# Kernel tuning notes

Hardware: AMD Instinct MI355X
Metric: run time of the kernel (lower is better)

Reference implementation:

```python
import jax, jax.numpy as jnp
import numpy as np

B, L, D, E, He = 8, 512, 300, 64, 64  # batch, seq_len, hidden_dim, edge_embed_dim, edge_hidden_dim


def setup_inputs() -> dict:
    key = jax.random.key(0)
    ks = jax.random.split(key, 7)
    return {
        "x": jax.random.normal(ks[0], (B, L, D), jnp.float32),
        "adj": jax.random.randint(ks[1], (B, L, L), 0, 2).astype(jnp.int32),
        "edge_embedding": jax.random.normal(ks[2], (B, L, L, E), jnp.float32),
        # learned params (xavier-ish scaling)
        "W_map": jax.random.normal(ks[3], (E, He), jnp.float32) / np.sqrt(E).astype(np.float32),
        "w_ew": jax.random.normal(ks[4], (He, 1), jnp.float32) / np.sqrt(He).astype(np.float32),
        "W_eto": jax.random.normal(ks[5], (D, D), jnp.float32) / np.sqrt(D).astype(np.float32),
        "b_eto": jnp.zeros((D,), jnp.float32),
    }


def reference(x, adj, edge_embedding, W_map, w_ew, W_eto, b_eto):
    # edge_mapping -> relu (dropout is identity in eval mode)
    em = jax.nn.relu(jnp.einsum('bije,eh->bijh', edge_embedding, W_map))  # [B,L,L,He]
    # edge_weight_liner (bias-free) -> [B,L,L]
    ew = jnp.einsum('bijh,ho->bij', em, w_ew)
    # row-wise abs-mean normalization (torch: mean(dim=-1).unsqueeze(-1), + 1e-10)
    row_mean = jnp.abs(jnp.mean(ew, axis=-1, keepdims=True)) + 1e-10
    ew = ew / row_mean
    # adjacency-masked softmax (torch uses -9e15 fill)
    scores = jnp.where(adj != 0, ew, jnp.float32(-9e15))
    att = jax.nn.softmax(scores, axis=-1)  # [B,L,L]
    # dense aggregation: edge_to(input) then attention matmul, relu
    h = x @ W_eto + b_eto  # [B,L,D]
    h_edge = jax.nn.relu(jnp.einsum('bij,bjd->bid', att, h))  # [B,L,D]
    return h_edge, att
```

## Files before the change

### kernel.cpp

```cpp
#include <hip/hip_runtime.h>
#include <hip/hip_bf16.h>

#define LSEQ 512
#define DDIM 300

typedef __attribute__((ext_vector_type(8))) short short8;
typedef __attribute__((ext_vector_type(4))) float f32x4;

__device__ __forceinline__ void split4(f32x4 v, short8& hi, short8& lo, int base) {
  #pragma unroll
  for (int e = 0; e < 4; ++e) {
    const float f = v[e];
    const unsigned b = __float_as_uint(f);
    const float hf = __uint_as_float(b & 0xffff0000u);
    hi[base + e] = (short)(b >> 16);
    lo[base + e] = (short)(__float_as_uint(f - hf) >> 16);
  }
}

__global__ __launch_bounds__(256, 3) void k_ew(
    const float* __restrict__ emb, const float* __restrict__ Wmap,
    const float* __restrict__ wew, float* __restrict__ ew) {
  __shared__ float lds[2][4][1024];
  const int tid = threadIdx.x;
  const int lane = tid & 63, wid = tid >> 6;
  const int c = lane & 15, g = lane >> 4;

  short8 whi[4][2], wlo[4][2];
  #pragma unroll
  for (int nt = 0; nt < 4; ++nt) {
    #pragma unroll
    for (int s = 0; s < 2; ++s) {
      #pragma unroll
      for (int e2 = 0; e2 < 2; ++e2) {
        f32x4 w;
        #pragma unroll
        for (int e = 0; e < 4; ++e)
          w[e] = Wmap[(32 * s + 8 * g + 4 * e2 + e) * 64 + 16 * nt + c];
        split4(w, whi[nt][s], wlo[nt][s], 4 * e2);
      }
    }
  }
  float wv2[4][4];
  #pragma unroll
  for (int nt = 0; nt < 4; ++nt)
    #pragma unroll
    for (int reg = 0; reg < 4; ++reg)
      wv2[nt][reg] = wew[16 * nt + 4 * g + reg];

  const size_t ebase = ((size_t)blockIdx.x * 4 + wid) * 128;
  const float* gbase = emb + (ebase << 6);

  float* const lb0 = &lds[0][wid][0];
  float* const lb1 = &lds[1][wid][0];

  int wwb[4];
  #pragma unroll
  for (int i = 0; i < 4; ++i)
    wwb[i] = ((i * 1024 + lane * 16) ^ ((((i & 1) * 4 + g) & 7) << 4)) >> 2;

  const int rw0 = (c * 256 + (((2 * g + 0) ^ (c & 7)) << 4)) >> 2;
  const int rw1 = (c * 256 + (((2 * g + 1) ^ (c & 7)) << 4)) >> 2;
  const int rw2 = (c * 256 + (((2 * g + 8) ^ (c & 7)) << 4)) >> 2;
  const int rw3 = (c * 256 + (((2 * g + 9) ^ (c & 7)) << 4)) >> 2;

  f32x4 q0 = *(const f32x4*)(gbase + 0 * 256 + lane * 4);
  f32x4 q1 = *(const f32x4*)(gbase + 1 * 256 + lane * 4);
  f32x4 q2 = *(const f32x4*)(gbase + 2 * 256 + lane * 4);
  f32x4 q3 = *(const f32x4*)(gbase + 3 * 256 + lane * 4);
  *(f32x4*)(lb0 + wwb[0]) = q0;
  *(f32x4*)(lb0 + wwb[1]) = q1;
  *(f32x4*)(lb0 + wwb[2]) = q2;
  *(f32x4*)(lb0 + wwb[3]) = q3;

  #pragma unroll 1
  for (int it = 0; it < 8; ++it) {
    if (it < 7) {
      const float* nt_ = gbase + (size_t)(it + 1) * 1024;
      q0 = *(const f32x4*)(nt_ + 0 * 256 + lane * 4);
      q1 = *(const f32x4*)(nt_ + 1 * 256 + lane * 4);
      q2 = *(const f32x4*)(nt_ + 2 * 256 + lane * 4);
      q3 = *(const f32x4*)(nt_ + 3 * 256 + lane * 4);
    }
    float* const rb = (it & 1) ? lb1 : lb0;
    const f32x4 a0 = *(const f32x4*)(rb + rw0);
    const f32x4 a1 = *(const f32x4*)(rb + rw1);
    const f32x4 a2 = *(const f32x4*)(rb + rw2);
    const f32x4 a3 = *(const f32x4*)(rb + rw3);

    short8 ehi[2], elo[2];
    split4(a0, ehi[0], elo[0], 0);
    split4(a1, ehi[0], elo[0], 4);
    split4(a2, ehi[1], elo[1], 0);
    split4(a3, ehi[1], elo[1], 4);

    f32x4 acc[4];
    #pragma unroll
    for (int nt = 0; nt < 4; ++nt) acc[nt] = (f32x4){0.f, 0.f, 0.f, 0.f};
    #pragma unroll
    for (int s = 0; s < 2; ++s) {
      #pragma unroll
      for (int nt = 0; nt < 4; ++nt) {
        acc[nt] = __builtin_amdgcn_mfma_f32_16x16x32_bf16(whi[nt][s], ehi[s], acc[nt], 0, 0, 0);
        acc[nt] = __builtin_amdgcn_mfma_f32_16x16x32_bf16(whi[nt][s], elo[s], acc[nt], 0, 0, 0);
        acc[nt] = __builtin_amdgcn_mfma_f32_16x16x32_bf16(wlo[nt][s], ehi[s], acc[nt], 0, 0, 0);
      }
    }
    float p = 0.f;
    #pragma unroll
    for (int nt = 0; nt < 4; ++nt)
      #pragma unroll
      for (int reg = 0; reg < 4; ++reg)
        p = fmaf(fmaxf(acc[nt][reg], 0.f), wv2[nt][reg], p);
    p += __shfl_xor(p, 16, 64);
    p += __shfl_xor(p, 32, 64);
    if (lane < 16) ew[ebase + it * 16 + c] = p;

    if (it < 7) {
      float* const wb = (it & 1) ? lb0 : lb1;
      *(f32x4*)(wb + wwb[0]) = q0;
      *(f32x4*)(wb + wwb[1]) = q1;
      *(f32x4*)(wb + wwb[2]) = q2;
      *(f32x4*)(wb + wwb[3]) = q3;
    }
  }
}

__global__ __launch_bounds__(256) void k_sm(
    const float* __restrict__ ew, const int* __restrict__ adj,
    float* __restrict__ att) {
  __shared__ float redA[4], redB[4], redC[4];
  const int tid = threadIdx.x;
  const int lane = tid & 63, wid = tid >> 6;
  const size_t rowbase = (size_t)blockIdx.x * LSEQ;

  const float ew0 = ew[rowbase + tid];
  const float ew1 = ew[rowbase + tid + 256];

  float ls = ew0 + ew1;
  #pragma unroll
  for (int m = 32; m >= 1; m >>= 1) ls += __shfl_xor(ls, m, 64);
  if (lane == 0) redA[wid] = ls;
  __syncthreads();
  const float rmean =
      fabsf((redA[0] + redA[1] + redA[2] + redA[3]) * (1.0f / 512.0f)) + 1e-10f;

  const int a0i = adj[rowbase + tid];
  const int a1i = adj[rowbase + tid + 256];
  const float sc0 = a0i ? (ew0 / rmean) : -9e15f;
  const float sc1 = a1i ? (ew1 / rmean) : -9e15f;

  float lm = fmaxf(sc0, sc1);
  #pragma unroll
  for (int m = 32; m >= 1; m >>= 1) lm = fmaxf(lm, __shfl_xor(lm, m, 64));
  if (lane == 0) redB[wid] = lm;
  __syncthreads();
  const float mx = fmaxf(fmaxf(redB[0], redB[1]), fmaxf(redB[2], redB[3]));

  const float e0 = expf(sc0 - mx);
  const float e1 = expf(sc1 - mx);
  float es = e0 + e1;
  #pragma unroll
  for (int m = 32; m >= 1; m >>= 1) es += __shfl_xor(es, m, 64);
  if (lane == 0) redC[wid] = es;
  __syncthreads();
  const float denom = redC[0] + redC[1] + redC[2] + redC[3];

  att[rowbase + tid] = e0 / denom;
  att[rowbase + tid + 256] = e1 / denom;
}

__global__ __launch_bounds__(256) void k_h(
    const float* __restrict__ x, const float* __restrict__ W,
    const float* __restrict__ bias, float* __restrict__ h) {
  const int tid = threadIdx.x;
  const int lane = tid & 63, wid = tid >> 6;
  const int c = lane & 15, g = lane >> 4;
  const int gt = blockIdx.x * 4 + wid;
  const int rt = gt / 19, dt = gt % 19;
  const int r0 = rt * 16, d0 = dt * 16;
  const int dc = min(d0 + c, DDIM - 1);
  const float* xr = x + (size_t)(r0 + c) * DDIM;

  f32x4 acc = {0.f, 0.f, 0.f, 0.f};
  #pragma unroll 3
  for (int ks = 0; ks < 9; ++ks) {
    const int k0 = ks * 32 + 8 * g;
    const f32x4 a0 = *(const f32x4*)(xr + k0);
    const f32x4 a1 = *(const f32x4*)(xr + k0 + 4);
    short8 ahi, alo;
    split4(a0, ahi, alo, 0);
    split4(a1, ahi, alo, 4);
    const float* wp = W + (size_t)k0 * DDIM + dc;
    const f32x4 b0 = {wp[0], wp[DDIM], wp[2 * DDIM], wp[3 * DDIM]};
    const f32x4 b1 = {wp[4 * DDIM], wp[5 * DDIM], wp[6 * DDIM], wp[7 * DDIM]};
    short8 bhi, blo;
    split4(b0, bhi, blo, 0);
    split4(b1, bhi, blo, 4);
    acc = __builtin_amdgcn_mfma_f32_16x16x32_bf16(ahi, bhi, acc, 0, 0, 0);
    acc = __builtin_amdgcn_mfma_f32_16x16x32_bf16(ahi, blo, acc, 0, 0, 0);
    acc = __builtin_amdgcn_mfma_f32_16x16x32_bf16(alo, bhi, acc, 0, 0, 0);
  }
  {
    float av[8], bv[8];
    #pragma unroll
    for (int e = 0; e < 8; ++e) {
      const int kk = 288 + 8 * g + e;
      const bool ok = kk < DDIM;
      av[e] = ok ? xr[kk] : 0.f;
      bv[e] = ok ? W[(size_t)kk * DDIM + dc] : 0.f;
    }
    const f32x4 a0 = {av[0], av[1], av[2], av[3]};
    const f32x4 a1 = {av[4], av[5], av[6], av[7]};
    const f32x4 b0 = {bv[0], bv[1], bv[2], bv[3]};
    const f32x4 b1 = {bv[4], bv[5], bv[6], bv[7]};
    short8 ahi, alo, bhi, blo;
    split4(a0, ahi, alo, 0);
    split4(a1, ahi, alo, 4);
    split4(b0, bhi, blo, 0);
    split4(b1, bhi, blo, 4);
    acc = __builtin_amdgcn_mfma_f32_16x16x32_bf16(ahi, bhi, acc, 0, 0, 0);
    acc = __builtin_amdgcn_mfma_f32_16x16x32_bf16(ahi, blo, acc, 0, 0, 0);
    acc = __builtin_amdgcn_mfma_f32_16x16x32_bf16(alo, bhi, acc, 0, 0, 0);
  }
  if (d0 + c < DDIM) {
    const float bb = bias[d0 + c];
    #pragma unroll
    for (int reg = 0; reg < 4; ++reg)
      h[(size_t)(r0 + 4 * g + reg) * DDIM + d0 + c] = acc[reg] + bb;
  }
}

__global__ __launch_bounds__(256) void k_out(
    const float* __restrict__ att, const float* __restrict__ h,
    float* __restrict__ out) {
  const int tid = threadIdx.x;
  const int lane = tid & 63, wid = tid >> 6;
  const int c = lane & 15, g = lane >> 4;
  const int gt = blockIdx.x * 4 + wid;
  const int b = gt / 608, rem = gt % 608;
  const int it = rem / 19, dt = rem % 19;
  const int i0 = it * 16, d0 = dt * 16;
  const int dc = min(d0 + c, DDIM - 1);
  const float* attR = att + ((size_t)b * LSEQ + i0 + c) * LSEQ + 8 * g;
  const float* hB = h + (size_t)b * LSEQ * DDIM;

  f32x4 acc = {0.f, 0.f, 0.f, 0.f};
  #pragma unroll 2
  for (int ks = 0; ks < 16; ++ks) {
    const int k0 = ks * 32;
    const f32x4 a0 = *(const f32x4*)(attR + k0);
    const f32x4 a1 = *(const f32x4*)(attR + k0 + 4);
    short8 ahi, alo;
    split4(a0, ahi, alo, 0);
    split4(a1, ahi, alo, 4);
    const float* hp = hB + (size_t)(k0 + 8 * g) * DDIM + dc;
    const f32x4 b0 = {hp[0], hp[DDIM], hp[2 * DDIM], hp[3 * DDIM]};
    const f32x4 b1 = {hp[4 * DDIM], hp[5 * DDIM], hp[6 * DDIM], hp[7 * DDIM]};
    short8 bhi, blo;
    split4(b0, bhi, blo, 0);
    split4(b1, bhi, blo, 4);
    acc = __builtin_amdgcn_mfma_f32_16x16x32_bf16(ahi, bhi, acc, 0, 0, 0);
    acc = __builtin_amdgcn_mfma_f32_16x16x32_bf16(ahi, blo, acc, 0, 0, 0);
    acc = __builtin_amdgcn_mfma_f32_16x16x32_bf16(alo, bhi, acc, 0, 0, 0);
  }
  if (d0 + c < DDIM) {
    #pragma unroll
    for (int reg = 0; reg < 4; ++reg)
      out[((size_t)b * LSEQ + i0 + 4 * g + reg) * DDIM + d0 + c] =
          fmaxf(acc[reg], 0.f);
  }
}

extern "C" void kernel_launch(void* const* d_in, const int* in_sizes, int n_in,
                              void* d_out, int out_size, void* d_ws, size_t ws_size,
                              hipStream_t stream) {
  const float* x    = (const float*)d_in[0];
  const int*   adj  = (const int*)d_in[1];
  const float* emb  = (const float*)d_in[2];
  const float* Wmap = (const float*)d_in[3];
  const float* wew  = (const float*)d_in[4];
  const float* Weto = (const float*)d_in[5];
  const float* beto = (const float*)d_in[6];

  float* out    = (float*)d_out;
  float* h_edge = out;
  float* att    = out + (size_t)8 * LSEQ * DDIM;
  float* ew     = (float*)d_ws;
  float* h      = ew + (size_t)8 * LSEQ * LSEQ;

  k_ew<<<dim3(4096), 256, 0, stream>>>(emb, Wmap, wew, ew);
  k_sm<<<dim3(4096), 256, 0, stream>>>(ew, adj, att);
  k_h<<<dim3(1216), 256, 0, stream>>>(x, Weto, beto, h);
  k_out<<<dim3(1216), 256, 0, stream>>>(att, h, h_edge);
}
```

Measured before the change: 160.8 us.

## Fuse edge-weight, softmax and h projection into one kernel; widen k_out tile

```diff
diff --git a/kernel.cpp b/kernel.cpp
--- a/kernel.cpp
+++ b/kernel.cpp
@@ -18,13 +18,75 @@
   }
 }
 
-__global__ __launch_bounds__(256, 3) void k_ew(
-    const float* __restrict__ emb, const float* __restrict__ Wmap,
-    const float* __restrict__ wew, float* __restrict__ ew) {
-  __shared__ float lds[2][4][1024];
+__global__ __launch_bounds__(256, 3) void k_fused1(
+    const float* __restrict__ emb, const int* __restrict__ adj,
+    const float* __restrict__ Wmap, const float* __restrict__ wew,
+    const float* __restrict__ x, const float* __restrict__ Weto,
+    const float* __restrict__ beto,
+    float* __restrict__ att, float* __restrict__ h) {
+  __shared__ float stg[2][4][1024];
+  __shared__ float ew_lds[LSEQ];
+  __shared__ float redA[4], redB[4], redC[4];
   const int tid = threadIdx.x;
   const int lane = tid & 63, wid = tid >> 6;
   const int c = lane & 15, g = lane >> 4;
+
+  if (blockIdx.x >= 4096) {
+    const int gt = (blockIdx.x - 4096) * 4 + wid;
+    const int rt = gt / 19, dt = gt % 19;
+    const int r0 = rt * 16, d0 = dt * 16;
+    const int dc = min(d0 + c, DDIM - 1);
+    const float* xr = x + (size_t)(r0 + c) * DDIM;
+
+    f32x4 acc = {0.f, 0.f, 0.f, 0.f};
+    #pragma unroll 3
+    for (int ks = 0; ks < 9; ++ks) {
+      const int k0 = ks * 32 + 8 * g;
+      const f32x4 a0 = *(const f32x4*)(xr + k0);
+      const f32x4 a1 = *(const f32x4*)(xr + k0 + 4);
+      short8 ahi, alo;
+      split4(a0, ahi, alo, 0);
+      split4(a1, ahi, alo, 4);
+      const float* wp = Weto + (size_t)k0 * DDIM + dc;
+      const f32x4 b0 = {wp[0], wp[DDIM], wp[2 * DDIM], wp[3 * DDIM]};
+      const f32x4 b1 = {wp[4 * DDIM], wp[5 * DDIM], wp[6 * DDIM], wp[7 * DDIM]};
+      short8 bhi, blo;
+      split4(b0, bhi, blo, 0);
+      split4(b1, bhi, blo, 4);
+      acc = __builtin_amdgcn_mfma_f32_16x16x32_bf16(ahi, bhi, acc, 0, 0, 0);
+      acc = __builtin_amdgcn_mfma_f32_16x16x32_bf16(ahi, blo, acc, 0, 0, 0);
+      acc = __builtin_amdgcn_mfma_f32_16x16x32_bf16(alo, bhi, acc, 0, 0, 0);
+    }
+    {
+      float av[8], bv[8];
+      #pragma unroll
+      for (int e = 0; e < 8; ++e) {
+        const int kk = 288 + 8 * g + e;
+        const bool ok = kk < DDIM;
+        av[e] = ok ? xr[kk] : 0.f;
+        bv[e] = ok ? Weto[(size_t)kk * DDIM + dc] : 0.f;
+      }
+      const f32x4 a0 = {av[0], av[1], av[2], av[3]};
+      const f32x4 a1 = {av[4], av[5], av[6], av[7]};
+      const f32x4 b0 = {bv[0], bv[1], bv[2], bv[3]};
+      const f32x4 b1 = {bv[4], bv[5], bv[6], bv[7]};
+      short8 ahi, alo, bhi, blo;
+      split4(a0, ahi, alo, 0);
+      split4(a1, ahi, alo, 4);
+      split4(b0, bhi, blo, 0);
+      split4(b1, bhi, blo, 4);
+      acc = __builtin_amdgcn_mfma_f32_16x16x32_bf16(ahi, bhi, acc, 0, 0, 0);
+      acc = __builtin_amdgcn_mfma_f32_16x16x32_bf16(ahi, blo, acc, 0, 0, 0);
+      acc = __builtin_amdgcn_mfma_f32_16x16x32_bf16(alo, bhi, acc, 0, 0, 0);
+    }
+    if (d0 + c < DDIM) {
+      const float bb = beto[d0 + c];
+      #pragma unroll
+      for (int reg = 0; reg < 4; ++reg)
+        h[(size_t)(r0 + 4 * g + reg) * DDIM + d0 + c] = acc[reg] + bb;
+    }
+    return;
+  }
 
   short8 whi[4][2], wlo[4][2];
   #pragma unroll
@@ -48,11 +110,12 @@
     for (int reg = 0; reg < 4; ++reg)
       wv2[nt][reg] = wew[16 * nt + 4 * g + reg];
 
-  const size_t ebase = ((size_t)blockIdx.x * 4 + wid) * 128;
+  const size_t rowbase = (size_t)blockIdx.x * LSEQ;
+  const size_t ebase = rowbase + (size_t)wid * 128;
   const float* gbase = emb + (ebase << 6);
 
-  float* const lb0 = &lds[0][wid][0];
-  float* const lb1 = &lds[1][wid][0];
+  float* const lb0 = &stg[0][wid][0];
+  float* const lb1 = &stg[1][wid][0];
 
   int wwb[4];
   #pragma unroll
@@ -114,7 +177,7 @@
         p = fmaf(fmaxf(acc[nt][reg], 0.f), wv2[nt][reg], p);
     p += __shfl_xor(p, 16, 64);
     p += __shfl_xor(p, 32, 64);
-    if (lane < 16) ew[ebase + it * 16 + c] = p;
+    if (lane < 16) ew_lds[wid * 128 + it * 16 + c] = p;
 
     if (it < 7) {
       float* const wb = (it & 1) ? lb0 : lb1;
@@ -124,18 +187,10 @@
       *(f32x4*)(wb + wwb[3]) = q3;
     }
   }
-}
-
-__global__ __launch_bounds__(256) void k_sm(
-    const float* __restrict__ ew, const int* __restrict__ adj,
-    float* __restrict__ att) {
-  __shared__ float redA[4], redB[4], redC[4];
-  const int tid = threadIdx.x;
-  const int lane = tid & 63, wid = tid >> 6;
-  const size_t rowbase = (size_t)blockIdx.x * LSEQ;
-
-  const float ew0 = ew[rowbase + tid];
-  const float ew1 = ew[rowbase + tid + 256];
+  __syncthreads();
+
+  const float ew0 = ew_lds[tid];
+  const float ew1 = ew_lds[tid + 256];
 
   float ls = ew0 + ew1;
   #pragma unroll
@@ -168,67 +223,6 @@
 
   att[rowbase + tid] = e0 / denom;
   att[rowbase + tid + 256] = e1 / denom;
-}
-
-__global__ __launch_bounds__(256) void k_h(
-    const float* __restrict__ x, const float* __restrict__ W,
-    const float* __restrict__ bias, float* __restrict__ h) {
-  const int tid = threadIdx.x;
-  const int lane = tid & 63, wid = tid >> 6;
-  const int c = lane & 15, g = lane >> 4;
-  const int gt = blockIdx.x * 4 + wid;
-  const int rt = gt / 19, dt = gt % 19;
-  const int r0 = rt * 16, d0 = dt * 16;
-  const int dc = min(d0 + c, DDIM - 1);
-  const float* xr = x + (size_t)(r0 + c) * DDIM;
-
-  f32x4 acc = {0.f, 0.f, 0.f, 0.f};
-  #pragma unroll 3
-  for (int ks = 0; ks < 9; ++ks) {
-    const int k0 = ks * 32 + 8 * g;
-    const f32x4 a0 = *(const f32x4*)(xr + k0);
-    const f32x4 a1 = *(const f32x4*)(xr + k0 + 4);
-    short8 ahi, alo;
-    split4(a0, ahi, alo, 0);
-    split4(a1, ahi, alo, 4);
-    const float* wp = W + (size_t)k0 * DDIM + dc;
-    const f32x4 b0 = {wp[0], wp[DDIM], wp[2 * DDIM], wp[3 * DDIM]};
-    const f32x4 b1 = {wp[4 * DDIM], wp[5 * DDIM], wp[6 * DDIM], wp[7 * DDIM]};
-    short8 bhi, blo;
-    split4(b0, bhi, blo, 0);
-    split4(b1, bhi, blo, 4);
-    acc = __builtin_amdgcn_mfma_f32_16x16x32_bf16(ahi, bhi, acc, 0, 0, 0);
-    acc = __builtin_amdgcn_mfma_f32_16x16x32_bf16(ahi, blo, acc, 0, 0, 0);
-    acc = __builtin_amdgcn_mfma_f32_16x16x32_bf16(alo, bhi, acc, 0, 0, 0);
-  }
-  {
-    float av[8], bv[8];
-    #pragma unroll
-    for (int e = 0; e < 8; ++e) {
-      const int kk = 288 + 8 * g + e;
-      const bool ok = kk < DDIM;
-      av[e] = ok ? xr[kk] : 0.f;
-      bv[e] = ok ? W[(size_t)kk * DDIM + dc] : 0.f;
-    }
-    const f32x4 a0 = {av[0], av[1], av[2], av[3]};
-    const f32x4 a1 = {av[4], av[5], av[6], av[7]};
-    const f32x4 b0 = {bv[0], bv[1], bv[2], bv[3]};
-    const f32x4 b1 = {bv[4], bv[5], bv[6], bv[7]};
-    short8 ahi, alo, bhi, blo;
-    split4(a0, ahi, alo, 0);
-    split4(a1, ahi, alo, 4);
-    split4(b0, bhi, blo, 0);
-    split4(b1, bhi, blo, 4);
-    acc = __builtin_amdgcn_mfma_f32_16x16x32_bf16(ahi, bhi, acc, 0, 0, 0);
-    acc = __builtin_amdgcn_mfma_f32_16x16x32_bf16(ahi, blo, acc, 0, 0, 0);
-    acc = __builtin_amdgcn_mfma_f32_16x16x32_bf16(alo, bhi, acc, 0, 0, 0);
-  }
-  if (d0 + c < DDIM) {
-    const float bb = bias[d0 + c];
-    #pragma unroll
-    for (int reg = 0; reg < 4; ++reg)
-      h[(size_t)(r0 + 4 * g + reg) * DDIM + d0 + c] = acc[reg] + bb;
-  }
 }
 
 __global__ __launch_bounds__(256) void k_out(
@@ -238,37 +232,49 @@
   const int lane = tid & 63, wid = tid >> 6;
   const int c = lane & 15, g = lane >> 4;
   const int gt = blockIdx.x * 4 + wid;
-  const int b = gt / 608, rem = gt % 608;
-  const int it = rem / 19, dt = rem % 19;
-  const int i0 = it * 16, d0 = dt * 16;
+  const int b = gt / 304, rem = gt % 304;
+  const int i2 = rem / 19, dt = rem % 19;
+  const int i0 = i2 * 32, d0 = dt * 16;
   const int dc = min(d0 + c, DDIM - 1);
-  const float* attR = att + ((size_t)b * LSEQ + i0 + c) * LSEQ + 8 * g;
+  const float* attR0 = att + ((size_t)b * LSEQ + i0 + c) * LSEQ + 8 * g;
+  const float* attR1 = attR0 + (size_t)16 * LSEQ;
   const float* hB = h + (size_t)b * LSEQ * DDIM;
 
-  f32x4 acc = {0.f, 0.f, 0.f, 0.f};
+  f32x4 acc0 = {0.f, 0.f, 0.f, 0.f};
+  f32x4 acc1 = {0.f, 0.f, 0.f, 0.f};
   #pragma unroll 2
   for (int ks = 0; ks < 16; ++ks) {
     const int k0 = ks * 32;
-    const f32x4 a0 = *(const f32x4*)(attR + k0);
-    const f32x4 a1 = *(const f32x4*)(attR + k0 + 4);
-    short8 ahi, alo;
-    split4(a0, ahi, alo, 0);
-    split4(a1, ahi, alo, 4);
+    const f32x4 a0 = *(const f32x4*)(attR0 + k0);
+    const f32x4 a1 = *(const f32x4*)(attR0 + k0 + 4);
+    const f32x4 a2 = *(const f32x4*)(attR1 + k0);
+    const f32x4 a3 = *(const f32x4*)(attR1 + k0 + 4);
+    short8 ahi0, alo0, ahi1, alo1;
+    split4(a0, ahi0, alo0, 0);
+    split4(a1, ahi0, alo0, 4);
+    split4(a2, ahi1, alo1, 0);
+    split4(a3, ahi1, alo1, 4);
     const float* hp = hB + (size_t)(k0 + 8 * g) * DDIM + dc;
     const f32x4 b0 = {hp[0], hp[DDIM], hp[2 * DDIM], hp[3 * DDIM]};
     const f32x4 b1 = {hp[4 * DDIM], hp[5 * DDIM], hp[6 * DDIM], hp[7 * DDIM]};
     short8 bhi, blo;
     split4(b0, bhi, blo, 0);
     split4(b1, bhi, blo, 4);
-    acc = __builtin_amdgcn_mfma_f32_16x16x32_bf16(ahi, bhi, acc, 0, 0, 0);
-    acc = __builtin_amdgcn_mfma_f32_16x16x32_bf16(ahi, blo, acc, 0, 0, 0);
-    acc = __builtin_amdgcn_mfma_f32_16x16x32_bf16(alo, bhi, acc, 0, 0, 0);
+    acc0 = __builtin_amdgcn_mfma_f32_16x16x32_bf16(ahi0, bhi, acc0, 0, 0, 0);
+    acc0 = __builtin_amdgcn_mfma_f32_16x16x32_bf16(ahi0, blo, acc0, 0, 0, 0);
+    acc0 = __builtin_amdgcn_mfma_f32_16x16x32_bf16(alo0, bhi, acc0, 0, 0, 0);
+    acc1 = __builtin_amdgcn_mfma_f32_16x16x32_bf16(ahi1, bhi, acc1, 0, 0, 0);
+    acc1 = __builtin_amdgcn_mfma_f32_16x16x32_bf16(ahi1, blo, acc1, 0, 0, 0);
+    acc1 = __builtin_amdgcn_mfma_f32_16x16x32_bf16(alo1, bhi, acc1, 0, 0, 0);
   }
   if (d0 + c < DDIM) {
     #pragma unroll
-    for (int reg = 0; reg < 4; ++reg)
+    for (int reg = 0; reg < 4; ++reg) {
       out[((size_t)b * LSEQ + i0 + 4 * g + reg) * DDIM + d0 + c] =
-          fmaxf(acc[reg], 0.f);
+          fmaxf(acc0[reg], 0.f);
+      out[((size_t)b * LSEQ + i0 + 16 + 4 * g + reg) * DDIM + d0 + c] =
+          fmaxf(acc1[reg], 0.f);
+    }
   }
 }
 
@@ -286,11 +292,9 @@
   float* out    = (float*)d_out;
   float* h_edge = out;
   float* att    = out + (size_t)8 * LSEQ * DDIM;
-  float* ew     = (float*)d_ws;
-  float* h      = ew + (size_t)8 * LSEQ * LSEQ;
-
-  k_ew<<<dim3(4096), 256, 0, stream>>>(emb, Wmap, wew, ew);
-  k_sm<<<dim3(4096), 256, 0, stream>>>(ew, adj, att);
-  k_h<<<dim3(1216), 256, 0, stream>>>(x, Weto, beto, h);
-  k_out<<<dim3(1216), 256, 0, stream>>>(att, h, h_edge);
+  float* h      = (float*)d_ws;
+
+  k_fused1<<<dim3(4096 + 1216), 256, 0, stream>>>(emb, adj, Wmap, wew, x, Weto,
+                                                  beto, att, h);
+  k_out<<<dim3(608), 256, 0, stream>>>(att, h, h_edge);
 }
```

Measured after the change: 145.5 us. -9.6%, faster.
